# Performance work log

Measured on AMD Instinct MI355X. Metric: run time of the kernel, lower is better.

## Reference

```python
import jax, jax.numpy as jnp
import numpy as np


def setup_inputs() -> dict:
    key = jax.random.key(0)
    k1, k2, k3 = jax.random.split(key, 3)
    x = jax.random.normal(k1, (16, 128, 128, 64), dtype=jnp.float32)
    kernel = jax.random.normal(k2, (3, 3, 64, 128), dtype=jnp.float32) * 0.05
    bias = jax.random.normal(k3, (128,), dtype=jnp.float32) * 0.05
    return {"x": x, "kernel": kernel, "bias": bias}


def reference(x, kernel, bias):
    # Faithful to myconv2d: extract_patches (stride 1, rate 1, SAME) followed by
    # per-out-channel multiply+reduce over the flattened (kh*kw*cin) patch axis,
    # which is mathematically a stride-1 SAME conv2d. Expressed as a direct conv.
    out = jax.lax.conv_general_dilated(
        x, kernel,
        window_strides=(1, 1),
        padding="SAME",
        dimension_numbers=("NHWC", "HWIO", "NHWC"),
    )
    return out + bias  # bias broadcast over channel dim, as in call()
```

## Files before the change

kernel.cpp:

```cpp
#include <hip/hip_runtime.h>


#define HH 128
#define WW 128
#define CIN 64
#define COUT 128

typedef __attribute__((ext_vector_type(8))) short v8s;
typedef __attribute__((ext_vector_type(4))) float v4f;

#define ROW_CHUNKS 528
#define WS_NEEDED  (9u * CIN * COUT * 2u)

static __device__ __forceinline__ unsigned short f2bf(float f) {
    unsigned int u = __float_as_uint(f);
    unsigned int r = (u + 0x7fffu + ((u >> 16) & 1u)) >> 16;
    return (unsigned short)r;
}

__global__ __launch_bounds__(256) void cvt_w(const float* __restrict__ wgt,
                                             unsigned short* __restrict__ wt) {
    int idx = blockIdx.x * 256 + threadIdx.x;
    if (idx >= 9 * CIN * COUT) return;
    int co  = idx & (COUT - 1);
    int ci  = (idx >> 7) & (CIN - 1);
    int tap = idx >> 13;
    int kc  = ci >> 5;
    int cl  = ci & 31;
    wt[((tap * 2 + kc) * COUT + co) * 32 + cl] = f2bf(wgt[idx]);
}

__global__ __launch_bounds__(256, 3) void conv_mfma(
    const float* __restrict__ x,
    const unsigned short* __restrict__ wt,
    const float* __restrict__ bias,
    float* __restrict__ out) {
    __shared__ v8s smem[3 * ROW_CHUNKS];

    int bid = blockIdx.x;
    int logical = ((bid & 7) << 9) | (bid >> 3);
    int wh = logical & 1;
    int h  = (logical >> 1) & (HH - 1);
    int n  = logical >> 8;
    int w0 = wh << 6;

    int tid  = threadIdx.x;
    int lane = tid & 63;
    int wid  = tid >> 6;
    int l15  = lane & 15;
    int quad = lane >> 4;

    #pragma unroll
    for (int dh = 0; dh < 3; ++dh) {
        int ih = h + dh - 1;
        bool rowok = (ih >= 0) && (ih < HH);
        const float* rowf = x + ((size_t)(n * HH + (rowok ? ih : 0))) * WW * CIN;
        v8s* dst = smem + dh * ROW_CHUNKS;
        #pragma unroll
        for (int k = 0; k < 3; ++k) {
            int c = tid + (k << 8);
            if (c < ROW_CHUNKS) {
                int lp = c >> 3;
                int gp = w0 - 1 + lp;
                v8s ch = (v8s)(short)0;
                if (rowok && gp >= 0 && gp < WW) {
                    const float* p = rowf + gp * CIN + (c & 7) * 8;
                    float4 a = *(const float4*)p;
                    float4 b = *(const float4*)(p + 4);
                    ch[0] = (short)f2bf(a.x); ch[1] = (short)f2bf(a.y);
                    ch[2] = (short)f2bf(a.z); ch[3] = (short)f2bf(a.w);
                    ch[4] = (short)f2bf(b.x); ch[5] = (short)f2bf(b.y);
                    ch[6] = (short)f2bf(b.z); ch[7] = (short)f2bf(b.w);
                }
                dst[c ^ (lp & 7)] = ch;
            }
        }
    }

    const unsigned short* wlane = wt + ((size_t)(wid * 32 + l15)) * 32 + quad * 8;
    v8s bb[3][2];
    #pragma unroll
    for (int tj = 0; tj < 2; ++tj) {
        bb[0][tj] = *(const v8s*)(wlane + 0 * 4096 + tj * 512);
        bb[1][tj] = *(const v8s*)(wlane + 1 * 4096 + tj * 512);
    }

    __syncthreads();

    v4f acc[4][2];
    #pragma unroll
    for (int i = 0; i < 4; ++i)
        #pragma unroll
        for (int j = 0; j < 2; ++j) acc[i][j] = (v4f)0.f;

    #pragma unroll
    for (int s = 0; s < 18; ++s) {
        const int tap = s >> 1;
        const int dh  = tap / 3;
        const int dw  = tap % 3;
        const int kc  = s & 1;
        const int cur = s % 3;

        if (s < 16) {
            const int nb = (s + 2) % 3;
            #pragma unroll
            for (int tj = 0; tj < 2; ++tj)
                bb[nb][tj] = *(const v8s*)(wlane + (s + 2) * 4096 + tj * 512);
        }

        const v8s* srow = smem + dh * ROW_CHUNKS;
        const int lp0 = l15 + dw;
        const int sw  = lp0 & 7;
        const int c0  = lp0 * 8 + kc * 4 + quad;

        v8s a0 = srow[(c0 + 0 * 128) ^ sw];
        v8s a1 = srow[(c0 + 1 * 128) ^ sw];
        #pragma unroll
        for (int tj = 0; tj < 2; ++tj)
            acc[0][tj] = __builtin_amdgcn_mfma_f32_16x16x32_bf16(
                a0, bb[cur][tj], acc[0][tj], 0, 0, 0);
        v8s a2 = srow[(c0 + 2 * 128) ^ sw];
        #pragma unroll
        for (int tj = 0; tj < 2; ++tj)
            acc[1][tj] = __builtin_amdgcn_mfma_f32_16x16x32_bf16(
                a1, bb[cur][tj], acc[1][tj], 0, 0, 0);
        v8s a3 = srow[(c0 + 3 * 128) ^ sw];
        #pragma unroll
        for (int tj = 0; tj < 2; ++tj)
            acc[2][tj] = __builtin_amdgcn_mfma_f32_16x16x32_bf16(
                a2, bb[cur][tj], acc[2][tj], 0, 0, 0);
        #pragma unroll
        for (int tj = 0; tj < 2; ++tj)
            acc[3][tj] = __builtin_amdgcn_mfma_f32_16x16x32_bf16(
                a3, bb[cur][tj], acc[3][tj], 0, 0, 0);
    }

    float bv[2];
    #pragma unroll
    for (int tj = 0; tj < 2; ++tj) bv[tj] = bias[wid * 32 + tj * 16 + l15];

    const float* __restrict__ ob =
        out + ((size_t)(n * HH + h) * WW + w0) * COUT + wid * 32 + l15;
    #pragma unroll
    for (int ti = 0; ti < 4; ++ti) {
        #pragma unroll
        for (int r = 0; r < 4; ++r) {
            int p = ti * 16 + quad * 4 + r;
            float* op = (float*)ob + (size_t)p * COUT;
            op[0]  = acc[ti][0][r] + bv[0];
            op[16] = acc[ti][1][r] + bv[1];
        }
    }
}

__global__ __launch_bounds__(256) void conv3x3_direct(
    const float* __restrict__ x, const float* __restrict__ wgt,
    const float* __restrict__ bias, float* __restrict__ out) {
    int idx = blockIdx.x * 256 + threadIdx.x;
    int co = idx & (COUT - 1);
    int w  = (idx >> 7) & (WW - 1);
    int h  = (idx >> 14) & (HH - 1);
    int n  = idx >> 21;
    float acc = bias[co];
    #pragma unroll
    for (int kh = 0; kh < 3; ++kh) {
        int ih = h + kh - 1;
        if (ih < 0 || ih >= HH) continue;
        #pragma unroll
        for (int kw = 0; kw < 3; ++kw) {
            int iw = w + kw - 1;
            if (iw < 0 || iw >= WW) continue;
            const float* xp = x + (((size_t)(n * HH + ih) * WW + iw) * CIN);
            const float* wp = wgt + ((size_t)((kh * 3 + kw) * CIN)) * COUT + co;
            #pragma unroll 8
            for (int ci = 0; ci < CIN; ++ci)
                acc = fmaf(xp[ci], wp[(size_t)ci * COUT], acc);
        }
    }
    out[idx] = acc;
}

extern "C" void kernel_launch(void* const* d_in, const int* in_sizes, int n_in,
                              void* d_out, int out_size, void* d_ws, size_t ws_size,
                              hipStream_t stream) {
    const float* x    = (const float*)d_in[0];
    const float* wgt  = (const float*)d_in[1];
    const float* bias = (const float*)d_in[2];
    float* out = (float*)d_out;

    if (ws_size < (size_t)WS_NEEDED) {
        int blocks = (out_size + 255) / 256;
        conv3x3_direct<<<blocks, 256, 0, stream>>>(x, wgt, bias, out);
        return;
    }

    unsigned short* wt = (unsigned short*)d_ws;
    cvt_w<<<(9 * CIN * COUT + 255) / 256, 256, 0, stream>>>(wgt, wt);
    conv_mfma<<<16 * HH * 2, 256, 0, stream>>>(x, wt, bias, out);
}
```

Baseline: 228.9 us.

## Preload all weight fragments into registers and double-buffer LDS A loads

All 18 steps of B (weight) fragments are loaded into 36 v8s registers at kernel start, issued before the input staging so their latency overlaps the global-to-LDS fill. The main loop now prefetches the next step's A fragments from LDS while the current step's MFMAs run. The bias load is also hoisted ahead of the barrier. This removes in-loop global weight loads but sharply raises VGPR use (about 144 registers for weights alone), so launch bounds drop from 3 to 2 waves per SIMD, which lowers occupancy.

```diff
diff --git a/kernel.cpp b/kernel.cpp
--- a/kernel.cpp
+++ b/kernel.cpp
@@ -30,7 +30,7 @@
     wt[((tap * 2 + kc) * COUT + co) * 32 + cl] = f2bf(wgt[idx]);
 }
 
-__global__ __launch_bounds__(256, 3) void conv_mfma(
+__global__ __launch_bounds__(256, 2) void conv_mfma(
     const float* __restrict__ x,
     const unsigned short* __restrict__ wt,
     const float* __restrict__ bias,
@@ -49,6 +49,14 @@
     int wid  = tid >> 6;
     int l15  = lane & 15;
     int quad = lane >> 4;
+
+    const unsigned short* wlane = wt + ((size_t)(wid * 32 + l15)) * 32 + quad * 8;
+    v8s breg[36];
+    #pragma unroll
+    for (int s = 0; s < 18; ++s) {
+        breg[2 * s]     = *(const v8s*)(wlane + s * 4096);
+        breg[2 * s + 1] = *(const v8s*)(wlane + s * 4096 + 512);
+    }
 
     #pragma unroll
     for (int dh = 0; dh < 3; ++dh) {
@@ -77,13 +85,9 @@
         }
     }
 
-    const unsigned short* wlane = wt + ((size_t)(wid * 32 + l15)) * 32 + quad * 8;
-    v8s bb[3][2];
-    #pragma unroll
-    for (int tj = 0; tj < 2; ++tj) {
-        bb[0][tj] = *(const v8s*)(wlane + 0 * 4096 + tj * 512);
-        bb[1][tj] = *(const v8s*)(wlane + 1 * 4096 + tj * 512);
-    }
+    float bv[2];
+    bv[0] = bias[wid * 32 + l15];
+    bv[1] = bias[wid * 32 + 16 + l15];
 
     __syncthreads();
 
@@ -93,51 +97,41 @@
         #pragma unroll
         for (int j = 0; j < 2; ++j) acc[i][j] = (v4f)0.f;
 
+#define LOADA(dst, ss) do {                                            \
+        const int tap_ = (ss) >> 1;                                    \
+        const int dh_  = tap_ / 3;                                     \
+        const int dw_  = tap_ % 3;                                     \
+        const int kc_  = (ss) & 1;                                     \
+        const v8s* srow_ = smem + dh_ * ROW_CHUNKS;                    \
+        const int lp0_ = l15 + dw_;                                    \
+        const int sw_  = lp0_ & 7;                                     \
+        const int c0_  = lp0_ * 8 + kc_ * 4 + quad;                    \
+        dst[0] = srow_[(c0_ + 0 * 128) ^ sw_];                         \
+        dst[1] = srow_[(c0_ + 1 * 128) ^ sw_];                         \
+        dst[2] = srow_[(c0_ + 2 * 128) ^ sw_];                         \
+        dst[3] = srow_[(c0_ + 3 * 128) ^ sw_];                         \
+    } while (0)
+
+    v8s ac[4], an[4];
+    LOADA(ac, 0);
     #pragma unroll
     for (int s = 0; s < 18; ++s) {
-        const int tap = s >> 1;
-        const int dh  = tap / 3;
-        const int dw  = tap % 3;
-        const int kc  = s & 1;
-        const int cur = s % 3;
+        if (s < 17) LOADA(an, s + 1);
 
-        if (s < 16) {
-            const int nb = (s + 2) % 3;
-            #pragma unroll
-            for (int tj = 0; tj < 2; ++tj)
-                bb[nb][tj] = *(const v8s*)(wlane + (s + 2) * 4096 + tj * 512);
+        #pragma unroll
+        for (int ti = 0; ti < 4; ++ti) {
+            acc[ti][0] = __builtin_amdgcn_mfma_f32_16x16x32_bf16(
+                ac[ti], breg[2 * s], acc[ti][0], 0, 0, 0);
+            acc[ti][1] = __builtin_amdgcn_mfma_f32_16x16x32_bf16(
+                ac[ti], breg[2 * s + 1], acc[ti][1], 0, 0, 0);
         }
 
-        const v8s* srow = smem + dh * ROW_CHUNKS;
-        const int lp0 = l15 + dw;
-        const int sw  = lp0 & 7;
-        const int c0  = lp0 * 8 + kc * 4 + quad;
-
-        v8s a0 = srow[(c0 + 0 * 128) ^ sw];
-        v8s a1 = srow[(c0 + 1 * 128) ^ sw];
-        #pragma unroll
-        for (int tj = 0; tj < 2; ++tj)
-            acc[0][tj] = __builtin_amdgcn_mfma_f32_16x16x32_bf16(
-                a0, bb[cur][tj], acc[0][tj], 0, 0, 0);
-        v8s a2 = srow[(c0 + 2 * 128) ^ sw];
-        #pragma unroll
-        for (int tj = 0; tj < 2; ++tj)
-            acc[1][tj] = __builtin_amdgcn_mfma_f32_16x16x32_bf16(
-                a1, bb[cur][tj], acc[1][tj], 0, 0, 0);
-        v8s a3 = srow[(c0 + 3 * 128) ^ sw];
-        #pragma unroll
-        for (int tj = 0; tj < 2; ++tj)
-            acc[2][tj] = __builtin_amdgcn_mfma_f32_16x16x32_bf16(
-                a2, bb[cur][tj], acc[2][tj], 0, 0, 0);
-        #pragma unroll
-        for (int tj = 0; tj < 2; ++tj)
-            acc[3][tj] = __builtin_amdgcn_mfma_f32_16x16x32_bf16(
-                a3, bb[cur][tj], acc[3][tj], 0, 0, 0);
+        if (s < 17) {
+            #pragma unroll
+            for (int t = 0; t < 4; ++t) ac[t] = an[t];
+        }
     }
-
-    float bv[2];
-    #pragma unroll
-    for (int tj = 0; tj < 2; ++tj) bv[tj] = bias[wid * 32 + tj * 16 + l15];
+#undef LOADA
 
     const float* __restrict__ ob =
         out + ((size_t)(n * HH + h) * WW + w0) * COUT + wid * 32 + l15;
```

After: 248.3 us. 1.08x slower.
